# Performance work log

Measured on AMD Instinct MI355X. Metric: run time of the kernel, lower is better.

The kernel has to match this reference:

```python
import jax, jax.numpy as jnp
import numpy as np

B, S, D = 32, 8192, 256

def setup_inputs() -> dict:
    key = jax.random.key(0)
    k1, k2 = jax.random.split(key)
    sequence = jax.random.normal(k1, (B, S, D), dtype=jnp.float32)
    vector = jax.random.normal(k2, (B, D), dtype=jnp.float32)
    sequence_mask = jnp.ones((B, S), dtype=jnp.float32)
    return {"sequence": sequence, "vector": vector, "sequence_mask": sequence_mask}

def _masked_softmax(logits, mask):
    # stable masked softmax: exp(logits - max) * mask, renormalized
    m = jnp.max(logits, axis=-1, keepdims=True)
    e = jnp.exp(logits - m) * mask
    return e / (jnp.sum(e, axis=-1, keepdims=True) + 1e-13)

def reference(sequence, vector, sequence_mask):
    # DotProduct similarity for every word at once (replaces the per-word loop)
    # scores: [B, S]
    scores = jnp.einsum('bsd,bd->bs', sequence, vector)
    attn = _masked_softmax(scores, sequence_mask)  # [B, S]
    # attention pooling: weighted sum over the sequence -> [B, D]
    pooled = jnp.einsum('bs,bsd->bd', attn, sequence)
    return (pooled, attn)
```

## Files before the change

### kernel.cpp

```cpp
#include <hip/hip_runtime.h>
#include <math.h>

constexpr int NB  = 32;
constexpr int NS  = 8192;
constexpr int ND  = 256;
constexpr int BPB = 64;
constexpr int RPB = NS / BPB;
constexpr int NWAVES = 4;
constexpr int RBATCH = 8;
constexpr int PSTRIDE = ND + 2;

__global__ __launch_bounds__(256) void k1_partial(
    const float* __restrict__ seq,
    const float* __restrict__ vec,
    const float* __restrict__ mask,
    float* __restrict__ scores,
    float* __restrict__ partials)
{
    const int blk   = blockIdx.x;
    const int b     = blk / BPB;
    const int chunk = blk % BPB;
    const int tid   = threadIdx.x;
    const int lane  = tid & 63;
    const int wave  = tid >> 6;

    const float4 v = *reinterpret_cast<const float4*>(vec + b * ND + lane * 4);

    float  m = -1e30f;
    float  l = 0.f;
    float4 o = make_float4(0.f, 0.f, 0.f, 0.f);

    const int row0 = chunk * RPB;
    const float* __restrict__ seqb   = seq  + (size_t)b * NS * ND;
    const float* __restrict__ maskb  = mask + (size_t)b * NS;
    float* __restrict__       scoreb = scores + (size_t)b * NS;

    for (int r0 = wave * RBATCH; r0 < RPB; r0 += NWAVES * RBATCH) {
        const int s0 = row0 + r0;
        float4 x[RBATCH];
        float  dot[RBATCH];
        #pragma unroll
        for (int k = 0; k < RBATCH; ++k)
            x[k] = *reinterpret_cast<const float4*>(seqb + (size_t)(s0 + k) * ND + lane * 4);
        #pragma unroll
        for (int k = 0; k < RBATCH; ++k)
            dot[k] = x[k].x * v.x + x[k].y * v.y + x[k].z * v.z + x[k].w * v.w;
        #pragma unroll
        for (int off = 32; off > 0; off >>= 1) {
            #pragma unroll
            for (int k = 0; k < RBATCH; ++k)
                dot[k] += __shfl_xor(dot[k], off, 64);
        }
        if (lane == 0) {
            *reinterpret_cast<float4*>(scoreb + s0)     = make_float4(dot[0], dot[1], dot[2], dot[3]);
            *reinterpret_cast<float4*>(scoreb + s0 + 4) = make_float4(dot[4], dot[5], dot[6], dot[7]);
        }
        const float4 mk0 = *reinterpret_cast<const float4*>(maskb + s0);
        const float4 mk1 = *reinterpret_cast<const float4*>(maskb + s0 + 4);

        const float mx = fmaxf(fmaxf(fmaxf(dot[0], dot[1]), fmaxf(dot[2], dot[3])),
                               fmaxf(fmaxf(dot[4], dot[5]), fmaxf(dot[6], dot[7])));
        const float mn    = fmaxf(m, mx);
        const float scale = __expf(m - mn);

        float e[RBATCH];
        e[0] = __expf(dot[0] - mn) * mk0.x;
        e[1] = __expf(dot[1] - mn) * mk0.y;
        e[2] = __expf(dot[2] - mn) * mk0.z;
        e[3] = __expf(dot[3] - mn) * mk0.w;
        e[4] = __expf(dot[4] - mn) * mk1.x;
        e[5] = __expf(dot[5] - mn) * mk1.y;
        e[6] = __expf(dot[6] - mn) * mk1.z;
        e[7] = __expf(dot[7] - mn) * mk1.w;

        l   *= scale;
        o.x *= scale; o.y *= scale; o.z *= scale; o.w *= scale;
        #pragma unroll
        for (int k = 0; k < RBATCH; ++k) {
            l   += e[k];
            o.x += e[k] * x[k].x;
            o.y += e[k] * x[k].y;
            o.z += e[k] * x[k].z;
            o.w += e[k] * x[k].w;
        }
        m = mn;
    }

    __shared__ float so[NWAVES][ND];
    __shared__ float sml[NWAVES][2];
    *reinterpret_cast<float4*>(&so[wave][lane * 4]) = o;
    if (lane == 0) { sml[wave][0] = m; sml[wave][1] = l; }
    __syncthreads();

    const float M = fmaxf(fmaxf(sml[0][0], sml[1][0]), fmaxf(sml[2][0], sml[3][0]));
    float L = 0.f, O = 0.f;
    #pragma unroll
    for (int w = 0; w < NWAVES; ++w) {
        const float wgt = __expf(sml[w][0] - M);
        L += sml[w][1] * wgt;
        O += so[w][tid] * wgt;
    }
    float* p = partials + (size_t)blk * PSTRIDE;
    p[tid] = O;
    if (tid == 0) { p[ND] = M; p[ND + 1] = L; }
}

__global__ __launch_bounds__(256) void k2_reduce(
    const float* __restrict__ partials,
    const float* __restrict__ mask,
    float* __restrict__ pooled,
    float* __restrict__ attn)
{
    const int b   = blockIdx.x;
    const int tid = threadIdx.x;
    __shared__ float w[BPB];
    __shared__ float sM, sL;
    const float* __restrict__ pb = partials + (size_t)b * BPB * PSTRIDE;

    if (tid < BPB) {
        const float mi = pb[tid * PSTRIDE + ND];
        float M = mi;
        #pragma unroll
        for (int off = 32; off > 0; off >>= 1)
            M = fmaxf(M, __shfl_xor(M, off, 64));
        const float li = pb[tid * PSTRIDE + ND + 1];
        const float wi = __expf(mi - M);
        w[tid] = wi;
        float L = li * wi;
        #pragma unroll
        for (int off = 32; off > 0; off >>= 1)
            L += __shfl_xor(L, off, 64);
        if (tid == 0) { sM = M; sL = L; }
    }
    __syncthreads();

    float acc = 0.f;
    #pragma unroll 8
    for (int i = 0; i < BPB; ++i)
        acc += pb[i * PSTRIDE + tid] * w[i];
    const float rL = 1.0f / (sL + 1e-13f);
    pooled[b * ND + tid] = acc * rL;

    const float M = sM;
    float4* __restrict__ ab = reinterpret_cast<float4*>(attn + (size_t)b * NS);
    const float4* __restrict__ mb = reinterpret_cast<const float4*>(mask + (size_t)b * NS);
    for (int i = tid; i < NS / 4; i += 256) {
        float4 sc = ab[i];
        const float4 mk = mb[i];
        sc.x = __expf(sc.x - M) * mk.x * rL;
        sc.y = __expf(sc.y - M) * mk.y * rL;
        sc.z = __expf(sc.z - M) * mk.z * rL;
        sc.w = __expf(sc.w - M) * mk.w * rL;
        ab[i] = sc;
    }
}

extern "C" void kernel_launch(void* const* d_in, const int* in_sizes, int n_in,
                              void* d_out, int out_size, void* d_ws, size_t ws_size,
                              hipStream_t stream)
{
    const float* seq  = (const float*)d_in[0];
    const float* vec  = (const float*)d_in[1];
    const float* mask = (const float*)d_in[2];

    float* pooled = (float*)d_out;
    float* attn   = pooled + NB * ND;

    float* partials = (float*)d_ws;

    k1_partial<<<NB * BPB, 256, 0, stream>>>(seq, vec, mask, attn, partials);
    k2_reduce<<<NB, 256, 0, stream>>>(partials, mask, pooled, attn);
}
```

Measured before the change: 53.35 us.

## Split waves into half-wave rows, double-buffer loads, move attn normalization to wide kernel

In the main partial kernel each half-wave now handles its own row with 8 floats per lane. Loads are double-buffered across a fully unrolled loop so the next batch of rows is in flight while the current one is processed. The final attention normalization, previously done by only 32 blocks in the reduce kernel, moves into a third kernel spread across many blocks. This adds a kernel launch and more live registers, in exchange for more memory-level parallelism and a parallel tail.

```diff
diff --git a/kernel.cpp b/kernel.cpp
--- a/kernel.cpp
+++ b/kernel.cpp
@@ -8,7 +8,9 @@
 constexpr int RPB = NS / BPB;
 constexpr int NWAVES = 4;
 constexpr int RBATCH = 8;
+constexpr int NITER  = RPB / (NWAVES * RBATCH);
 constexpr int PSTRIDE = ND + 2;
+constexpr int NPART = NWAVES * 2;
 
 __global__ __launch_bounds__(256) void k1_partial(
     const float* __restrict__ seq,
@@ -23,82 +25,105 @@
     const int tid   = threadIdx.x;
     const int lane  = tid & 63;
     const int wave  = tid >> 6;
-
-    const float4 v = *reinterpret_cast<const float4*>(vec + b * ND + lane * 4);
+    const int h     = lane >> 5;
+    const int sl    = lane & 31;
+
+    const float* vb = vec + b * ND + sl * 8;
+    const float4 v0 = *reinterpret_cast<const float4*>(vb);
+    const float4 v1 = *reinterpret_cast<const float4*>(vb + 4);
 
     float  m = -1e30f;
     float  l = 0.f;
-    float4 o = make_float4(0.f, 0.f, 0.f, 0.f);
+    float4 o0 = make_float4(0.f, 0.f, 0.f, 0.f);
+    float4 o1 = make_float4(0.f, 0.f, 0.f, 0.f);
 
     const int row0 = chunk * RPB;
     const float* __restrict__ seqb   = seq  + (size_t)b * NS * ND;
     const float* __restrict__ maskb  = mask + (size_t)b * NS;
     float* __restrict__       scoreb = scores + (size_t)b * NS;
 
-    for (int r0 = wave * RBATCH; r0 < RPB; r0 += NWAVES * RBATCH) {
-        const int s0 = row0 + r0;
-        float4 x[RBATCH];
-        float  dot[RBATCH];
-        #pragma unroll
-        for (int k = 0; k < RBATCH; ++k)
-            x[k] = *reinterpret_cast<const float4*>(seqb + (size_t)(s0 + k) * ND + lane * 4);
-        #pragma unroll
-        for (int k = 0; k < RBATCH; ++k)
-            dot[k] = x[k].x * v.x + x[k].y * v.y + x[k].z * v.z + x[k].w * v.w;
-        #pragma unroll
-        for (int off = 32; off > 0; off >>= 1) {
+    const int   sbase = row0 + wave * RBATCH + h * 4;
+    const float* base = seqb + (size_t)sbase * ND + sl * 8;
+
+    float4 xa0[4], xa1[4], xb0[4], xb1[4];
+
+    auto LOAD = [&](float4 (&x0)[4], float4 (&x1)[4], int it) {
+        const float* p = base + (size_t)it * (NWAVES * RBATCH) * ND;
+        #pragma unroll
+        for (int k = 0; k < 4; ++k) {
+            x0[k] = *reinterpret_cast<const float4*>(p + (size_t)k * ND);
+            x1[k] = *reinterpret_cast<const float4*>(p + (size_t)k * ND + 4);
+        }
+    };
+
+    auto PROC = [&](const float4 (&x0)[4], const float4 (&x1)[4], int it) {
+        float dot[4];
+        #pragma unroll
+        for (int k = 0; k < 4; ++k)
+            dot[k] = x0[k].x * v0.x + x0[k].y * v0.y + x0[k].z * v0.z + x0[k].w * v0.w
+                   + x1[k].x * v1.x + x1[k].y * v1.y + x1[k].z * v1.z + x1[k].w * v1.w;
+        #pragma unroll
+        for (int off = 1; off < 32; off <<= 1) {
             #pragma unroll
-            for (int k = 0; k < RBATCH; ++k)
+            for (int k = 0; k < 4; ++k)
                 dot[k] += __shfl_xor(dot[k], off, 64);
         }
-        if (lane == 0) {
-            *reinterpret_cast<float4*>(scoreb + s0)     = make_float4(dot[0], dot[1], dot[2], dot[3]);
-            *reinterpret_cast<float4*>(scoreb + s0 + 4) = make_float4(dot[4], dot[5], dot[6], dot[7]);
-        }
-        const float4 mk0 = *reinterpret_cast<const float4*>(maskb + s0);
-        const float4 mk1 = *reinterpret_cast<const float4*>(maskb + s0 + 4);
-
-        const float mx = fmaxf(fmaxf(fmaxf(dot[0], dot[1]), fmaxf(dot[2], dot[3])),
-                               fmaxf(fmaxf(dot[4], dot[5]), fmaxf(dot[6], dot[7])));
-        const float mn    = fmaxf(m, mx);
+        const int s0h = sbase + it * (NWAVES * RBATCH);
+        if (sl == 0)
+            *reinterpret_cast<float4*>(scoreb + s0h) =
+                make_float4(dot[0], dot[1], dot[2], dot[3]);
+        const float4 mk = *reinterpret_cast<const float4*>(maskb + s0h);
+
+        const float mx = fmaxf(fmaxf(dot[0], dot[1]), fmaxf(dot[2], dot[3]));
+        const float mn = fmaxf(m, mx);
         const float scale = __expf(m - mn);
-
-        float e[RBATCH];
-        e[0] = __expf(dot[0] - mn) * mk0.x;
-        e[1] = __expf(dot[1] - mn) * mk0.y;
-        e[2] = __expf(dot[2] - mn) * mk0.z;
-        e[3] = __expf(dot[3] - mn) * mk0.w;
-        e[4] = __expf(dot[4] - mn) * mk1.x;
-        e[5] = __expf(dot[5] - mn) * mk1.y;
-        e[6] = __expf(dot[6] - mn) * mk1.z;
-        e[7] = __expf(dot[7] - mn) * mk1.w;
-
-        l   *= scale;
-        o.x *= scale; o.y *= scale; o.z *= scale; o.w *= scale;
-        #pragma unroll
-        for (int k = 0; k < RBATCH; ++k) {
-            l   += e[k];
-            o.x += e[k] * x[k].x;
-            o.y += e[k] * x[k].y;
-            o.z += e[k] * x[k].z;
-            o.w += e[k] * x[k].w;
+        float e[4];
+        e[0] = __expf(dot[0] - mn) * mk.x;
+        e[1] = __expf(dot[1] - mn) * mk.y;
+        e[2] = __expf(dot[2] - mn) * mk.z;
+        e[3] = __expf(dot[3] - mn) * mk.w;
+        l    = l    * scale + e[0] + e[1] + e[2] + e[3];
+        o0.x = o0.x * scale; o0.y = o0.y * scale; o0.z = o0.z * scale; o0.w = o0.w * scale;
+        o1.x = o1.x * scale; o1.y = o1.y * scale; o1.z = o1.z * scale; o1.w = o1.w * scale;
+        #pragma unroll
+        for (int k = 0; k < 4; ++k) {
+            o0.x += e[k] * x0[k].x; o0.y += e[k] * x0[k].y;
+            o0.z += e[k] * x0[k].z; o0.w += e[k] * x0[k].w;
+            o1.x += e[k] * x1[k].x; o1.y += e[k] * x1[k].y;
+            o1.z += e[k] * x1[k].z; o1.w += e[k] * x1[k].w;
         }
         m = mn;
+    };
+
+    LOAD(xa0, xa1, 0);
+    #pragma unroll
+    for (int it = 0; it < NITER; ++it) {
+        if ((it & 1) == 0) {
+            if (it + 1 < NITER) LOAD(xb0, xb1, it + 1);
+            PROC(xa0, xa1, it);
+        } else {
+            if (it + 1 < NITER) LOAD(xa0, xa1, it + 1);
+            PROC(xb0, xb1, it);
+        }
     }
 
-    __shared__ float so[NWAVES][ND];
-    __shared__ float sml[NWAVES][2];
-    *reinterpret_cast<float4*>(&so[wave][lane * 4]) = o;
-    if (lane == 0) { sml[wave][0] = m; sml[wave][1] = l; }
+    __shared__ float so[NPART][ND];
+    __shared__ float sml[NPART][2];
+    const int u = wave * 2 + h;
+    *reinterpret_cast<float4*>(&so[u][sl * 8])     = o0;
+    *reinterpret_cast<float4*>(&so[u][sl * 8 + 4]) = o1;
+    if (sl == 0) { sml[u][0] = m; sml[u][1] = l; }
     __syncthreads();
 
-    const float M = fmaxf(fmaxf(sml[0][0], sml[1][0]), fmaxf(sml[2][0], sml[3][0]));
+    float M = sml[0][0];
+    #pragma unroll
+    for (int i = 1; i < NPART; ++i) M = fmaxf(M, sml[i][0]);
     float L = 0.f, O = 0.f;
     #pragma unroll
-    for (int w = 0; w < NWAVES; ++w) {
-        const float wgt = __expf(sml[w][0] - M);
-        L += sml[w][1] * wgt;
-        O += so[w][tid] * wgt;
+    for (int i = 0; i < NPART; ++i) {
+        const float wgt = __expf(sml[i][0] - M);
+        L += sml[i][1] * wgt;
+        O += so[i][tid] * wgt;
     }
     float* p = partials + (size_t)blk * PSTRIDE;
     p[tid] = O;
@@ -107,9 +132,8 @@
 
 __global__ __launch_bounds__(256) void k2_reduce(
     const float* __restrict__ partials,
-    const float* __restrict__ mask,
     float* __restrict__ pooled,
-    float* __restrict__ attn)
+    float* __restrict__ finals)
 {
     const int b   = blockIdx.x;
     const int tid = threadIdx.x;
@@ -140,19 +164,26 @@
         acc += pb[i * PSTRIDE + tid] * w[i];
     const float rL = 1.0f / (sL + 1e-13f);
     pooled[b * ND + tid] = acc * rL;
-
-    const float M = sM;
-    float4* __restrict__ ab = reinterpret_cast<float4*>(attn + (size_t)b * NS);
-    const float4* __restrict__ mb = reinterpret_cast<const float4*>(mask + (size_t)b * NS);
-    for (int i = tid; i < NS / 4; i += 256) {
-        float4 sc = ab[i];
-        const float4 mk = mb[i];
-        sc.x = __expf(sc.x - M) * mk.x * rL;
-        sc.y = __expf(sc.y - M) * mk.y * rL;
-        sc.z = __expf(sc.z - M) * mk.z * rL;
-        sc.w = __expf(sc.w - M) * mk.w * rL;
-        ab[i] = sc;
-    }
+    if (tid == 0) { finals[b * 2] = sM; finals[b * 2 + 1] = sL; }
+}
+
+__global__ __launch_bounds__(256) void k3_norm(
+    float* __restrict__ attn,
+    const float* __restrict__ mask,
+    const float* __restrict__ finals)
+{
+    const int idx = blockIdx.x * 256 + threadIdx.x;
+    const int i4  = idx * 4;
+    const int b   = i4 >> 13;
+    const float M  = finals[b * 2];
+    const float rL = 1.0f / (finals[b * 2 + 1] + 1e-13f);
+    float4 sc = *reinterpret_cast<float4*>(attn + i4);
+    const float4 mk = *reinterpret_cast<const float4*>(mask + i4);
+    sc.x = __expf(sc.x - M) * mk.x * rL;
+    sc.y = __expf(sc.y - M) * mk.y * rL;
+    sc.z = __expf(sc.z - M) * mk.z * rL;
+    sc.w = __expf(sc.w - M) * mk.w * rL;
+    *reinterpret_cast<float4*>(attn + i4) = sc;
 }
 
 extern "C" void kernel_launch(void* const* d_in, const int* in_sizes, int n_in,
@@ -167,7 +198,9 @@
     float* attn   = pooled + NB * ND;
 
     float* partials = (float*)d_ws;
+    float* finals   = partials + (size_t)NB * BPB * PSTRIDE;
 
     k1_partial<<<NB * BPB, 256, 0, stream>>>(seq, vec, mask, attn, partials);
-    k2_reduce<<<NB, 256, 0, stream>>>(partials, mask, pooled, attn);
-}
+    k2_reduce<<<NB, 256, 0, stream>>>(partials, pooled, finals);
+    k3_norm<<<NB * NS / (256 * 4), 256, 0, stream>>>(attn, mask, finals);
+}
```

New measurement: 51.78 us. -2.9%, faster.
